# Performance work log

Hardware: AMD Instinct MI355X
Metric: run time of the kernel (lower is better)

## Reference

```python
import jax, jax.numpy as jnp
import numpy as np

DIM = 384
HEADS = 8


def setup_inputs() -> dict:
    key = jax.random.key(0)
    k_x, k_qkv, k_pw, k_pb = jax.random.split(key, 4)
    x = jax.random.normal(k_x, (8, DIM, 32, 32), dtype=jnp.float32)
    # Conv2d 1x1 weights stored as [out, in]
    w_qkv = jax.random.normal(k_qkv, (3 * DIM, DIM), dtype=jnp.float32) * (DIM ** -0.5)
    w_proj = jax.random.normal(k_pw, (DIM, DIM), dtype=jnp.float32) * (DIM ** -0.5)
    b_proj = jax.random.normal(k_pb, (DIM,), dtype=jnp.float32) * 0.02
    return {"x": x, "w_qkv": w_qkv, "w_proj": w_proj, "b_proj": b_proj}


def reference(x, w_qkv, w_proj, b_proj):
    B, C, H, W = x.shape
    h = HEADS
    d = C // h
    scale = d ** -0.5
    # 1x1 conv == channel-wise linear: [B,3C,H,W]
    qkv = jnp.einsum('oc,bchw->bohw', w_qkv, x)
    q, k, v = jnp.split(qkv, 3, axis=1)
    # B (h d) H W -> B h (H W) d
    def to_heads(y):
        return y.reshape(B, h, d, H * W).transpose(0, 1, 3, 2)
    q, k, v = to_heads(q), to_heads(k), to_heads(v)
    att = jnp.einsum('bhxd,bhyd->bhxy', q * scale, k)
    att = jax.nn.softmax(att, axis=-1)
    out = jnp.einsum('bhxy,bhyd->bhxd', att, v)
    # B h (H W) d -> B (h d) H W
    out = out.transpose(0, 1, 3, 2).reshape(B, C, H, W)
    out = jnp.einsum('oc,bchw->bohw', w_proj, out) + b_proj[None, :, None, None]
    return out
```

## Files before the change

kernel.cpp:

```cpp
#include <hip/hip_runtime.h>
#include <math.h>

typedef unsigned short u16;
typedef __attribute__((ext_vector_type(8))) short short8;
typedef __attribute__((ext_vector_type(8))) unsigned short ushort8;
typedef __attribute__((ext_vector_type(4))) float floatx4;
typedef __attribute__((ext_vector_type(2))) unsigned int uint2v;

#define SEQ 1024
#define CDIM 384
#define NH 8
#define DH 48
#define DP 64
#define NB 8

__device__ __forceinline__ u16 f2bf(float f){
  unsigned int u; __builtin_memcpy(&u, &f, 4);
  u = (u + 0x7fffu + ((u >> 16) & 1u)) >> 16;
  return (u16)u;
}
__device__ __forceinline__ unsigned packbf(float a, float b){
  unsigned ua, ub; __builtin_memcpy(&ua, &a, 4); __builtin_memcpy(&ub, &b, 4);
  ua += 0x7fffu + ((ua >> 16) & 1u);
  ub += 0x7fffu + ((ub >> 16) & 1u);
  return __builtin_amdgcn_perm(ub, ua, 0x07060302);
}
__device__ __forceinline__ void async16(const u16* g, u16* l){
  __builtin_amdgcn_global_load_lds((const __attribute__((address_space(1))) void*)g,
                                   (__attribute__((address_space(3))) void*)l, 16, 0, 0);
}

__global__ __launch_bounds__(256) void prep_kernel(const float* __restrict__ x,
                                                   const float* __restrict__ wq,
                                                   const float* __restrict__ wp,
                                                   u16* __restrict__ xT,
                                                   u16* __restrict__ wdst){
  __shared__ u16 ldsT[64 * 72];
  const int id = blockIdx.x;
  const int t = threadIdx.x;
  if (id < 768){
    const int bx = id & 15, by = (id >> 4) % 6, bz = id / 96;
    const int c0 = by * 64;
    const int s0 = bx * 64;
    const int rr = t >> 2, q4 = t & 3;

    const float* src = x + ((size_t)(bz * CDIM + c0 + rr)) * SEQ + s0;
#pragma unroll
    for (int i = 0; i < 4; i++){
      const int cc = q4 + i * 4;
      float4 f = *(const float4*)(src + cc * 4);
      ldsT[(cc * 4 + 0) * 72 + rr] = f2bf(f.x);
      ldsT[(cc * 4 + 1) * 72 + rr] = f2bf(f.y);
      ldsT[(cc * 4 + 2) * 72 + rr] = f2bf(f.z);
      ldsT[(cc * 4 + 3) * 72 + rr] = f2bf(f.w);
    }
    __syncthreads();
    u16* dst = xT + ((size_t)(bz * SEQ + s0 + rr)) * CDIM + c0 + q4 * 16;
    *(ushort8*)(dst)     = *(const ushort8*)&ldsT[rr * 72 + q4 * 16];
    *(ushort8*)(dst + 8) = *(const ushort8*)&ldsT[rr * 72 + q4 * 16 + 8];
  } else {
    const int NWQ = 3 * CDIM * CDIM;
    const int i = ((id - 768) * 256 + t) * 4;
    const float* src = (i < NWQ) ? (wq + i) : (wp + (i - NWQ));
    float4 f = *(const float4*)src;
    uint2v v; v[0] = packbf(f.x, f.y); v[1] = packbf(f.z, f.w);
    *(uint2v*)(wdst + i) = v;
  }
}

__global__ __launch_bounds__(256) void qkv_kernel(const u16* __restrict__ W,
                                                  const u16* __restrict__ xT,
                                                  u16* __restrict__ qws,
                                                  u16* __restrict__ kws,
                                                  u16* __restrict__ vws){
  __shared__ u16 ldsA[128 * 64];
  __shared__ u16 ldsB[64 * 64];
  const int t = threadIdx.x;
  const int w = t >> 6, l = t & 63;
  const int quad = l >> 4, li = l & 15;
  const int n0 = blockIdx.x * 64;
  const int m0 = blockIdx.y * 128;
  const int b  = blockIdx.z;

  floatx4 acc[2][4];
#pragma unroll
  for (int i = 0; i < 2; i++)
#pragma unroll
    for (int j = 0; j < 4; j++) acc[i][j] = (floatx4)0.0f;

  const u16* xb = xT + (size_t)b * SEQ * CDIM;
  const int swz = li & 7;

  for (int kk = 0; kk < CDIM; kk += 64){
    __syncthreads();
#pragma unroll
    for (int rep = 0; rep < 4; rep++){
      const int cs = rep * 256 + t;
      const int row = cs >> 3, c4 = cs & 7;
      async16(&W[(size_t)(m0 + row) * CDIM + kk + ((c4 ^ (row & 7)) << 3)], &ldsA[cs * 8]);
    }
#pragma unroll
    for (int rep = 0; rep < 2; rep++){
      const int cs = rep * 256 + t;
      const int row = cs >> 3, c4 = cs & 7;
      async16(&xb[(size_t)(n0 + row) * CDIM + kk + ((c4 ^ (row & 7)) << 3)], &ldsB[cs * 8]);
    }
    __syncthreads();
#pragma unroll
    for (int kc = 0; kc < 2; kc++){
      const int rc = ((kc * 4 + quad) ^ swz) << 3;
      short8 af[2], bf[4];
#pragma unroll
      for (int i = 0; i < 2; i++)
        af[i] = *(const short8*)&ldsA[(w * 32 + i * 16 + li) * 64 + rc];
#pragma unroll
      for (int j = 0; j < 4; j++)
        bf[j] = *(const short8*)&ldsB[(j * 16 + li) * 64 + rc];
#pragma unroll
      for (int i = 0; i < 2; i++)
#pragma unroll
        for (int j = 0; j < 4; j++)
          acc[i][j] = __builtin_amdgcn_mfma_f32_16x16x32_bf16(af[i], bf[j], acc[i][j], 0, 0, 0);
    }
  }

  const float qs = 0.14433756729740643f * 1.4426950408889634f;
  const uint2v z2 = (uint2v)0u;
#pragma unroll
  for (int i = 0; i < 2; i++){
    const int obase = m0 + w * 32 + i * 16 + quad * 4;
    const int which = obase / CDIM;
    const int rem = obase - which * CDIM;
    const int h = rem / DH;
    const int dd = rem - h * DH;
    const int pair = b * NH + h;
#pragma unroll
    for (int j = 0; j < 4; j++){
      const int s = n0 + j * 16 + li;
      floatx4 v = acc[i][j];
      if (which == 0){
        uint2v pk; pk[0] = packbf(v[0] * qs, v[1] * qs); pk[1] = packbf(v[2] * qs, v[3] * qs);
        *(uint2v*)&qws[((size_t)pair * SEQ + s) * DP + dd] = pk;
        if ((dd & 48) == 32)
          *(uint2v*)&qws[((size_t)pair * SEQ + s) * DP + dd + 16] = z2;
      } else if (which == 1){
        uint2v pk; pk[0] = packbf(v[0], v[1]); pk[1] = packbf(v[2], v[3]);
        *(uint2v*)&kws[((size_t)pair * SEQ + s) * DP + dd] = pk;
        if ((dd & 48) == 32)
          *(uint2v*)&kws[((size_t)pair * SEQ + s) * DP + dd + 16] = z2;
      } else {
#pragma unroll
        for (int r = 0; r < 4; r++)
          vws[((size_t)pair * DH + dd + r) * SEQ + s] = f2bf(v[r]);
      }
    }
  }
}

__global__ __launch_bounds__(256) void attn_kernel(const u16* __restrict__ qws,
                                                   const u16* __restrict__ kws,
                                                   const u16* __restrict__ vws,
                                                   u16* __restrict__ aT){
  __shared__ u16 ldsK[2][64 * 64];
  __shared__ u16 ldsV[2][48 * 64];
  __shared__ u16 ldsP[64 * 72];

  const int t = threadIdx.x;
  const int w = t >> 6, l = t & 63;
  const int quad = l >> 4, li = l & 15;
  const int id = blockIdx.x;
  const int pair = id & 63;
  const int qb = id >> 6;
  const int b = pair >> 3, h = pair & 7;
  const int qbase = qb * 64 + w * 16;
  const int swz = li & 7;

  const u16* qrow = qws + ((size_t)pair * SEQ + qbase + li) * DP;
  const short8 qf0 = *(const short8*)(qrow + quad * 8);
  const short8 qf1 = *(const short8*)(qrow + 32 + quad * 8);

  floatx4 ot[3];
#pragma unroll
  for (int dt = 0; dt < 3; dt++) ot[dt] = (floatx4)0.0f;
  float m_run = -3.0e38f, l_run = 0.0f;

  const u16* kbase = kws + (size_t)pair * SEQ * DP;
  const u16* vbase = vws + (size_t)pair * DH * SEQ;

  auto stage = [&](int kv, int pp){
#pragma unroll
    for (int rep = 0; rep < 4; rep++){
      const int cs = rep * 256 + t;
      if (cs < 512){
        const int row = cs >> 3, c4 = cs & 7;
        async16(&kbase[(size_t)(kv + row) * DP + ((c4 ^ (row & 7)) << 3)],
                &ldsK[pp][cs * 8]);
      } else if (cs < 896){
        const int cs2 = cs - 512;
        const int row = cs2 >> 3, c4 = cs2 & 7;
        async16(&vbase[(size_t)row * SEQ + kv + ((c4 ^ (row & 7)) << 3)],
                &ldsV[pp][cs2 * 8]);
      }
    }
  };

  u16* prow = ldsP + (w * 16 + li) * 72;

  stage(0, 0);
  for (int i = 0; i < 16; i++){
    const int p = i & 1;
    __syncthreads();
    if (i < 15) stage((i + 1) * 64, p ^ 1);

    floatx4 st[4];
#pragma unroll
    for (int yt = 0; yt < 4; yt++){
      const u16* krow = ldsK[p] + (yt * 16 + li) * 64;
      const short8 kf0 = *(const short8*)(krow + (((0 + quad) ^ swz) << 3));
      const short8 kf1 = *(const short8*)(krow + (((4 + quad) ^ swz) << 3));
      floatx4 z = (floatx4)0.0f;
      z = __builtin_amdgcn_mfma_f32_16x16x32_bf16(kf0, qf0, z, 0, 0, 0);
      z = __builtin_amdgcn_mfma_f32_16x16x32_bf16(kf1, qf1, z, 0, 0, 0);
      st[yt] = z;
    }

    float mx = -3.0e38f;
#pragma unroll
    for (int yt = 0; yt < 4; yt++)
#pragma unroll
      for (int r = 0; r < 4; r++) mx = fmaxf(mx, st[yt][r]);
    mx = fmaxf(mx, __shfl_xor(mx, 16, 64));
    mx = fmaxf(mx, __shfl_xor(mx, 32, 64));
    const float mnew = fmaxf(m_run, mx);
    const float alpha = __builtin_amdgcn_exp2f(m_run - mnew);
    m_run = mnew;

    float ls = 0.0f;
#pragma unroll
    for (int yt = 0; yt < 4; yt++){
      float p0 = __builtin_amdgcn_exp2f(st[yt][0] - mnew);
      float p1 = __builtin_amdgcn_exp2f(st[yt][1] - mnew);
      float p2 = __builtin_amdgcn_exp2f(st[yt][2] - mnew);
      float p3 = __builtin_amdgcn_exp2f(st[yt][3] - mnew);
      ls += (p0 + p1) + (p2 + p3);
      uint2v pk; pk[0] = packbf(p0, p1); pk[1] = packbf(p2, p3);
      *(uint2v*)&prow[yt * 16 + quad * 4] = pk;
    }
    l_run = l_run * alpha + ls;
#pragma unroll
    for (int dt = 0; dt < 3; dt++) ot[dt] *= alpha;

#pragma unroll
    for (int ks = 0; ks < 64; ks += 32){
      const short8 pb = *(const short8*)&ldsP[(w * 16 + li) * 72 + ks + quad * 8];
#pragma unroll
      for (int dt = 0; dt < 3; dt++){
        const short8 vf = *(const short8*)&ldsV[p][(dt * 16 + li) * 64 +
                                                  ((((ks >> 3) + quad) ^ swz) << 3)];
        ot[dt] = __builtin_amdgcn_mfma_f32_16x16x32_bf16(vf, pb, ot[dt], 0, 0, 0);
      }
    }
  }

  float ls = l_run;
  ls += __shfl_xor(ls, 16, 64);
  ls += __shfl_xor(ls, 32, 64);
  const float rl = __builtin_amdgcn_rcpf(ls);
  const int q = qbase + li;
#pragma unroll
  for (int dt = 0; dt < 3; dt++){
    floatx4 v = ot[dt];
    uint2v pk; pk[0] = packbf(v[0] * rl, v[1] * rl); pk[1] = packbf(v[2] * rl, v[3] * rl);
    *(uint2v*)&aT[((size_t)b * SEQ + q) * CDIM + h * DH + dt * 16 + quad * 4] = pk;
  }
}

__global__ __launch_bounds__(256) void proj_kernel(const u16* __restrict__ W,
                                                   const u16* __restrict__ aT,
                                                   const float* __restrict__ bias,
                                                   float* __restrict__ out){
  __shared__ u16 ldsA[128 * 64];
  __shared__ u16 ldsB[64 * 64];
  const int t = threadIdx.x;
  const int w = t >> 6, l = t & 63;
  const int quad = l >> 4, li = l & 15;
  const int n0 = blockIdx.x * 64;
  const int m0 = blockIdx.y * 128;
  const int b  = blockIdx.z;

  floatx4 acc[2][4];
#pragma unroll
  for (int i = 0; i < 2; i++)
#pragma unroll
    for (int j = 0; j < 4; j++) acc[i][j] = (floatx4)0.0f;

  const u16* ab = aT + (size_t)b * SEQ * CDIM;
  const int swz = li & 7;

  for (int kk = 0; kk < CDIM; kk += 64){
    __syncthreads();
#pragma unroll
    for (int rep = 0; rep < 4; rep++){
      const int cs = rep * 256 + t;
      const int row = cs >> 3, c4 = cs & 7;
      async16(&W[(size_t)(m0 + row) * CDIM + kk + ((c4 ^ (row & 7)) << 3)], &ldsA[cs * 8]);
    }
#pragma unroll
    for (int rep = 0; rep < 2; rep++){
      const int cs = rep * 256 + t;
      const int row = cs >> 3, c4 = cs & 7;
      async16(&ab[(size_t)(n0 + row) * CDIM + kk + ((c4 ^ (row & 7)) << 3)], &ldsB[cs * 8]);
    }
    __syncthreads();
#pragma unroll
    for (int kc = 0; kc < 2; kc++){
      const int rc = ((kc * 4 + quad) ^ swz) << 3;
      short8 af[2], bf[4];
#pragma unroll
      for (int i = 0; i < 2; i++)
        af[i] = *(const short8*)&ldsA[(w * 32 + i * 16 + li) * 64 + rc];
#pragma unroll
      for (int j = 0; j < 4; j++)
        bf[j] = *(const short8*)&ldsB[(j * 16 + li) * 64 + rc];
#pragma unroll
      for (int i = 0; i < 2; i++)
#pragma unroll
        for (int j = 0; j < 4; j++)
          acc[i][j] = __builtin_amdgcn_mfma_f32_16x16x32_bf16(af[i], bf[j], acc[i][j], 0, 0, 0);
    }
  }

#pragma unroll
  for (int i = 0; i < 2; i++){
    const int o0 = m0 + w * 32 + i * 16 + quad * 4;
    float bs[4];
#pragma unroll
    for (int r = 0; r < 4; r++) bs[r] = bias[o0 + r];
#pragma unroll
    for (int j = 0; j < 4; j++){
      const int s = n0 + j * 16 + li;
#pragma unroll
      for (int r = 0; r < 4; r++)
        out[((size_t)b * CDIM + o0 + r) * SEQ + s] = acc[i][j][r] + bs[r];
    }
  }
}

extern "C" void kernel_launch(void* const* d_in, const int* in_sizes, int n_in,
                              void* d_out, int out_size, void* d_ws, size_t ws_size,
                              hipStream_t stream) {
  const float* x      = (const float*)d_in[0];
  const float* w_qkv  = (const float*)d_in[1];
  const float* w_proj = (const float*)d_in[2];
  const float* b_proj = (const float*)d_in[3];
  float* out = (float*)d_out;

  char* ws = (char*)d_ws;
  const size_t SZX = (size_t)NB * SEQ * CDIM * sizeof(u16);
  const size_t SZQ = (size_t)NB * NH * SEQ * DP * sizeof(u16);
  const size_t SZV = (size_t)NB * NH * SEQ * DH * sizeof(u16);
  u16* xT   = (u16*)(ws);
  u16* qws  = (u16*)(ws + SZX);
  u16* kws  = (u16*)(ws + SZX + SZQ);
  u16* vws  = (u16*)(ws + SZX + 2 * SZQ);
  u16* wq_b = (u16*)(ws + SZX + 2 * SZQ + SZV);
  u16* wp_b = wq_b + (size_t)3 * CDIM * CDIM;
  u16* aT   = xT;

  prep_kernel<<<dim3(768 + 576), 256, 0, stream>>>(x, w_qkv, w_proj, xT, wq_b);
  qkv_kernel<<<dim3(16, 9, 8), 256, 0, stream>>>(wq_b, xT, qws, kws, vws);
  attn_kernel<<<dim3(1024), 256, 0, stream>>>(qws, kws, vws, aT);
  proj_kernel<<<dim3(16, 3, 8), 256, 0, stream>>>(wp_b, aT, b_proj, out);
}
```

Before: 128.7 us.

## Keep attention probabilities in registers via permlane swaps and skip rescaling

Replaces the LDS round trip for the softmax probability tile with in-register reshuffling using v_permlane32/16_swap, so P feeds the PV MFMA directly. It also adds a lazy rescale that only updates the running max and rescales the accumulators when some lane's max grows by more than 11 (log2 units). The manual bf16 rounding is replaced by the hardware v_cvt_pk_bf16_f32 instruction everywhere, and attn_kernel gets a min-blocks launch bound of 4. The lazy rescale lets exponents reach up to 2^11 before renormalisation, which stays safe in fp32. The permlane layout must match the MFMA B-operand layout exactly, or the results will be wrong.

```diff
diff --git a/kernel.cpp b/kernel.cpp
--- a/kernel.cpp
+++ b/kernel.cpp
@@ -6,6 +6,7 @@
 typedef __attribute__((ext_vector_type(8))) unsigned short ushort8;
 typedef __attribute__((ext_vector_type(4))) float floatx4;
 typedef __attribute__((ext_vector_type(2))) unsigned int uint2v;
+typedef __attribute__((ext_vector_type(4))) unsigned int uint4v;
 
 #define SEQ 1024
 #define CDIM 384
@@ -19,11 +20,16 @@
   u = (u + 0x7fffu + ((u >> 16) & 1u)) >> 16;
   return (u16)u;
 }
-__device__ __forceinline__ unsigned packbf(float a, float b){
-  unsigned ua, ub; __builtin_memcpy(&ua, &a, 4); __builtin_memcpy(&ub, &b, 4);
-  ua += 0x7fffu + ((ua >> 16) & 1u);
-  ub += 0x7fffu + ((ub >> 16) & 1u);
-  return __builtin_amdgcn_perm(ub, ua, 0x07060302);
+__device__ __forceinline__ unsigned cvtpk(float a, float b){
+  unsigned r;
+  asm("v_cvt_pk_bf16_f32 %0, %1, %2" : "=v"(r) : "v"(a), "v"(b));
+  return r;
+}
+__device__ __forceinline__ void plswap32(unsigned &a, unsigned &b){
+  asm("v_permlane32_swap_b32 %0, %1" : "+v"(a), "+v"(b));
+}
+__device__ __forceinline__ void plswap16(unsigned &a, unsigned &b){
+  asm("v_permlane16_swap_b32 %0, %1" : "+v"(a), "+v"(b));
 }
 __device__ __forceinline__ void async16(const u16* g, u16* l){
   __builtin_amdgcn_global_load_lds((const __attribute__((address_space(1))) void*)g,
@@ -63,7 +69,7 @@
     const int i = ((id - 768) * 256 + t) * 4;
     const float* src = (i < NWQ) ? (wq + i) : (wp + (i - NWQ));
     float4 f = *(const float4*)src;
-    uint2v v; v[0] = packbf(f.x, f.y); v[1] = packbf(f.z, f.w);
+    uint2v v; v[0] = cvtpk(f.x, f.y); v[1] = cvtpk(f.z, f.w);
     *(uint2v*)(wdst + i) = v;
   }
 }
@@ -139,12 +145,12 @@
       const int s = n0 + j * 16 + li;
       floatx4 v = acc[i][j];
       if (which == 0){
-        uint2v pk; pk[0] = packbf(v[0] * qs, v[1] * qs); pk[1] = packbf(v[2] * qs, v[3] * qs);
+        uint2v pk; pk[0] = cvtpk(v[0] * qs, v[1] * qs); pk[1] = cvtpk(v[2] * qs, v[3] * qs);
         *(uint2v*)&qws[((size_t)pair * SEQ + s) * DP + dd] = pk;
         if ((dd & 48) == 32)
           *(uint2v*)&qws[((size_t)pair * SEQ + s) * DP + dd + 16] = z2;
       } else if (which == 1){
-        uint2v pk; pk[0] = packbf(v[0], v[1]); pk[1] = packbf(v[2], v[3]);
+        uint2v pk; pk[0] = cvtpk(v[0], v[1]); pk[1] = cvtpk(v[2], v[3]);
         *(uint2v*)&kws[((size_t)pair * SEQ + s) * DP + dd] = pk;
         if ((dd & 48) == 32)
           *(uint2v*)&kws[((size_t)pair * SEQ + s) * DP + dd + 16] = z2;
@@ -157,13 +163,12 @@
   }
 }
 
-__global__ __launch_bounds__(256) void attn_kernel(const u16* __restrict__ qws,
-                                                   const u16* __restrict__ kws,
-                                                   const u16* __restrict__ vws,
-                                                   u16* __restrict__ aT){
+__global__ __launch_bounds__(256, 4) void attn_kernel(const u16* __restrict__ qws,
+                                                      const u16* __restrict__ kws,
+                                                      const u16* __restrict__ vws,
+                                                      u16* __restrict__ aT){
   __shared__ u16 ldsK[2][64 * 64];
   __shared__ u16 ldsV[2][48 * 64];
-  __shared__ u16 ldsP[64 * 72];
 
   const int t = threadIdx.x;
   const int w = t >> 6, l = t & 63;
@@ -204,8 +209,6 @@
     }
   };
 
-  u16* prow = ldsP + (w * 16 + li) * 72;
-
   stage(0, 0);
   for (int i = 0; i < 16; i++){
     const int p = i & 1;
@@ -227,36 +230,45 @@
     float mx = -3.0e38f;
 #pragma unroll
     for (int yt = 0; yt < 4; yt++)
-#pragma unroll
-      for (int r = 0; r < 4; r++) mx = fmaxf(mx, st[yt][r]);
+      mx = fmaxf(mx, fmaxf(fmaxf(st[yt][0], st[yt][1]), fmaxf(st[yt][2], st[yt][3])));
     mx = fmaxf(mx, __shfl_xor(mx, 16, 64));
     mx = fmaxf(mx, __shfl_xor(mx, 32, 64));
-    const float mnew = fmaxf(m_run, mx);
-    const float alpha = __builtin_amdgcn_exp2f(m_run - mnew);
-    m_run = mnew;
-
+
+    if (!__all(mx - m_run <= 11.0f)){
+      const float mnew = fmaxf(m_run, mx);
+      const float alpha = __builtin_amdgcn_exp2f(m_run - mnew);
+      m_run = mnew;
+      l_run *= alpha;
+#pragma unroll
+      for (int dt = 0; dt < 3; dt++) ot[dt] *= alpha;
+    }
+
+    unsigned wv[4][2];
     float ls = 0.0f;
 #pragma unroll
     for (int yt = 0; yt < 4; yt++){
-      float p0 = __builtin_amdgcn_exp2f(st[yt][0] - mnew);
-      float p1 = __builtin_amdgcn_exp2f(st[yt][1] - mnew);
-      float p2 = __builtin_amdgcn_exp2f(st[yt][2] - mnew);
-      float p3 = __builtin_amdgcn_exp2f(st[yt][3] - mnew);
+      float p0 = __builtin_amdgcn_exp2f(st[yt][0] - m_run);
+      float p1 = __builtin_amdgcn_exp2f(st[yt][1] - m_run);
+      float p2 = __builtin_amdgcn_exp2f(st[yt][2] - m_run);
+      float p3 = __builtin_amdgcn_exp2f(st[yt][3] - m_run);
       ls += (p0 + p1) + (p2 + p3);
-      uint2v pk; pk[0] = packbf(p0, p1); pk[1] = packbf(p2, p3);
-      *(uint2v*)&prow[yt * 16 + quad * 4] = pk;
-    }
-    l_run = l_run * alpha + ls;
-#pragma unroll
-    for (int dt = 0; dt < 3; dt++) ot[dt] *= alpha;
-
-#pragma unroll
-    for (int ks = 0; ks < 64; ks += 32){
-      const short8 pb = *(const short8*)&ldsP[(w * 16 + li) * 72 + ks + quad * 8];
+      wv[yt][0] = cvtpk(p0, p1);
+      wv[yt][1] = cvtpk(p2, p3);
+    }
+    l_run += ls;
+
+#pragma unroll
+    for (int kh = 0; kh < 2; kh++){
+      unsigned d0 = wv[2 * kh][0],     d1 = wv[2 * kh][1];
+      unsigned e0 = wv[2 * kh + 1][0], e1 = wv[2 * kh + 1][1];
+      plswap32(d0, e0); plswap16(d0, e0);
+      plswap32(d1, e1); plswap16(d1, e1);
+      uint4v u; u[0] = d0; u[1] = d1; u[2] = e0; u[3] = e1;
+      const short8 pb = __builtin_bit_cast(short8, u);
 #pragma unroll
       for (int dt = 0; dt < 3; dt++){
         const short8 vf = *(const short8*)&ldsV[p][(dt * 16 + li) * 64 +
-                                                  ((((ks >> 3) + quad) ^ swz) << 3)];
+                                                  (((kh * 4 + quad) ^ swz) << 3)];
         ot[dt] = __builtin_amdgcn_mfma_f32_16x16x32_bf16(vf, pb, ot[dt], 0, 0, 0);
       }
     }
@@ -270,7 +282,7 @@
 #pragma unroll
   for (int dt = 0; dt < 3; dt++){
     floatx4 v = ot[dt];
-    uint2v pk; pk[0] = packbf(v[0] * rl, v[1] * rl); pk[1] = packbf(v[2] * rl, v[3] * rl);
+    uint2v pk; pk[0] = cvtpk(v[0] * rl, v[1] * rl); pk[1] = cvtpk(v[2] * rl, v[3] * rl);
     *(uint2v*)&aT[((size_t)b * SEQ + q) * CDIM + h * DH + dt * 16 + quad * 4] = pk;
   }
 }
```

New measurement: 122.7 us. -4.7%, faster.
